# Kernel tuning notes

Measured on AMD Instinct MI355X. Metric: run time of the kernel, lower is better.

Reference implementation:

```python
import jax, jax.numpy as jnp
import numpy as np

BS = 256          # batch_size
NN = BS - 1
D = 128           # projection dim
SIGMA = 0.07      # rbf gamma (self.sigma)
C = 1.0
REG = 0.1
NUM_ITERS = 1000
ETA = 0.001
USE_NORM = True


def setup_inputs() -> dict:
    key = jax.random.key(0)
    k1, k2 = jax.random.split(key)
    z = jax.random.normal(k1, (BS, 2, D), dtype=jnp.float32)
    alpha_init = jax.random.normal(k2, (BS, NN, 1), dtype=jnp.float32)
    return {"z": z, "alpha_init": alpha_init}


def _rbf_kernel(X, Y, gamma):
    # exp(-gamma * ||x - y||^2)
    xn = jnp.sum(X * X, axis=1, keepdims=True)          # [n,1]
    yn = jnp.sum(Y * Y, axis=1, keepdims=True).T        # [1,m]
    d = xn + yn - 2.0 * (X @ Y.T)
    return jnp.exp(-gamma * d)


def _pgd_nesterov(DD, p, alpha0, eta, num_iters, C, use_norm):
    # minimize 0.5 a'DDa - p'a  s.t. 0 <= a <= C, batched over bs
    def step(carry, t):
        alpha, alpha_prev = carry
        beta = t / (t + 3.0)
        y = alpha + beta * (alpha - alpha_prev)
        grad = jnp.einsum('bij,bjk->bik', DD, y) - p     # [bs,nn,1]
        if use_norm:
            grad = grad / (jnp.linalg.norm(grad, axis=1, keepdims=True) + 1e-12)
        alpha_new = jnp.clip(y - eta * grad, 0.0, C)
        return (alpha_new, alpha), None
    (alpha, _), _ = jax.lax.scan(step, (alpha0, alpha0),
                                 jnp.arange(num_iters, dtype=jnp.float32))
    return alpha


def reference(z, alpha_init):
    bs, nn = BS, NN
    # F.normalize(z, p=2, dim=1): normalize over the view axis (faithful to source)
    nrm = jnp.maximum(jnp.linalg.norm(z, axis=1, keepdims=True), 1e-12)
    ftr = z / nrm
    ftr = jnp.concatenate([ftr[:, 0, :], ftr[:, 1, :]], axis=0)   # [2bs, d]

    K = _rbf_kernel(ftr[:bs], ftr, SIGMA)                          # [bs, 2bs]

    # ---- QP construction + solve under no_grad ----
    Kd = jax.lax.stop_gradient(K)
    KK = Kd[:, :bs]                                                # block: first bs cols
    r = jnp.arange(bs)
    m = jnp.arange(nn)
    # idx[i] = [0..bs-1] without i  (KMASK row/col removal)
    idx = m[None, :] + (m[None, :] >= r[:, None]).astype(jnp.int32)  # [bs, nn]
    KK_sub = KK[idx[:, :, None], idx[:, None, :]]                  # [bs,nn,nn]
    row = jnp.take_along_axis(KK, idx, axis=1)                     # row[i,m]=KK[i,idx[i,m]]
    # Delta[i,j,k] = 1 + reg*d_jk + KK[j,k] - KK[i,j] - KK[i,k]  (j,k != i)
    DD = (1.0 + REG * jnp.eye(nn, dtype=KK.dtype)[None]
          + KK_sub - row[:, :, None] - row[:, None, :])            # [bs,nn,nn]

    p = 2.0 * jnp.ones((bs, nn, 1), dtype=jnp.float32)
    alpha0 = jnp.clip(jax.nn.relu(alpha_init), 0.0, C)
    alpha = _pgd_nesterov(DD, p, alpha0, ETA, NUM_ITERS, C, USE_NORM)
    alpha_y = jnp.clip(jax.nn.relu(alpha[:, :, 0]), 0.0, C)
    alpha_y = jax.lax.stop_gradient(alpha_y)                       # [bs,nn]
    alpha_x = alpha_y.sum(axis=1)                                  # [bs]

    # ---- loss terms (grad flows through K here) ----
    Ks = K[:, bs:]                                                 # block12: [bs,bs]
    # Kn.T[i,m] = Ks.T[i, idx[i,m]]  (neg_mask = off-diagonal)
    KnT = jnp.take_along_axis(Ks.T, idx, axis=1)                   # [bs,nn]
    pos = jnp.diagonal(Ks)                                         # pos_mask = eye
    pos_loss = jnp.mean(alpha_x * pos)
    neg_loss = jnp.sum(alpha_y * KnT) / bs
    loss = neg_loss - pos_loss

    sparsity = ((alpha_y == C).sum().astype(jnp.float32)
                / ((alpha_y > 0).sum().astype(jnp.float32) + 1e-10))
    num_zero = (alpha_y == 0.0).mean()
    return (loss, pos.mean(), KnT.mean(), sparsity, num_zero, jnp.float32(0.0))
```

## Files before the change

kernel.cpp:

```cpp
#include <hip/hip_runtime.h>
#include <math.h>

#define BS   256
#define NN   255
#define DIM  128
#define GAMMA 0.07
#define NUM_ITERS 1000

typedef float v2f __attribute__((ext_vector_type(2)));

__device__ __forceinline__ double wred_d(double v) {
  #pragma unroll
  for (int k = 1; k < 64; k <<= 1) v += __shfl_xor(v, k, 64);
  return v;
}
__device__ __forceinline__ int wred_i(int v) {
  #pragma unroll
  for (int k = 1; k < 64; k <<= 1) v += __shfl_xor(v, k, 64);
  return v;
}

__device__ __forceinline__ float RLF(float v, int lane) {
  return __int_as_float(__builtin_amdgcn_readlane(__float_as_int(v), lane));
}

template <int CTRL, int RMASK>
__device__ __forceinline__ float dpp_add(float x) {
  int t = __builtin_amdgcn_update_dpp(0, __float_as_int(x), CTRL, RMASK, 0xf, true);
  return x + __int_as_float(t);
}
__device__ __forceinline__ float wred64_dpp(float x) {
  x = dpp_add<0x111, 0xf>(x);
  x = dpp_add<0x112, 0xf>(x);
  x = dpp_add<0x114, 0xf>(x);
  x = dpp_add<0x118, 0xf>(x);
  x = dpp_add<0x142, 0xa>(x);
  x = dpp_add<0x143, 0xc>(x);
  return RLF(x, 63);
}

__device__ __forceinline__ float rsq_nr(float x) {
  float r;
  asm("v_rsq_f32 %0, %1" : "=v"(r) : "v"(x));
  r = r * (1.5f - 0.5f * x * r * r);
  return r;
}

__device__ __forceinline__ void pk_fma(v2f& acc, const v2f& k, const v2f& y) {
  asm("v_pk_fma_f32 %0, %1, %2, %0" : "+v"(acc) : "v"(k), "v"(y));
}

__device__ __forceinline__ float4 add4(float4 a, float4 b) {
  float4 c; c.x = a.x + b.x; c.y = a.y + b.y; c.z = a.z + b.z; c.w = a.w + b.w;
  return c;
}

__global__ void k_ftr(const float* __restrict__ z, double* __restrict__ ftrT) {
  int b = blockIdx.x;
  int d = threadIdx.x;
  double z0 = (double)z[b * 256 + d];
  double z1 = (double)z[b * 256 + 128 + d];
  double n = sqrt(z0 * z0 + z1 * z1);
  n = fmax(n, 1e-12);
  ftrT[d * 512 + b]       = z0 / n;
  ftrT[d * 512 + 256 + b] = z1 / n;
}

__global__ void k_K(const double* __restrict__ ftrT, float* __restrict__ K,
                    double* __restrict__ pk_knt, double* __restrict__ pos_arr) {
  int i = blockIdx.x;
  int t = threadIdx.x;
  __shared__ double rowi[DIM];
  __shared__ double redd[4];
  if (t < DIM) rowi[t] = ftrT[t * 512 + i];
  __syncthreads();
  double xn = 0.0;
  #pragma unroll 8
  for (int d = 0; d < DIM; ++d) xn += rowi[d] * rowi[d];

  double knt_part = 0.0;
  #pragma unroll
  for (int h = 0; h < 2; ++h) {
    int j = t + h * 256;
    double dot = 0.0, sq = 0.0;
    #pragma unroll 8
    for (int d = 0; d < DIM; ++d) {
      double f = ftrT[d * 512 + j];
      dot += rowi[d] * f;
      sq  += f * f;
    }
    double dist = xn + sq - 2.0 * dot;
    double kv = exp(-GAMMA * dist);
    K[i * 512 + j] = (float)kv;
    if (h == 1) {
      if (j == 256 + i) pos_arr[i] = kv;
      else knt_part += kv;
    }
  }
  double w = wred_d(knt_part);
  if ((t & 63) == 0) redd[t >> 6] = w;
  __syncthreads();
  if (t == 0) pk_knt[i] = redd[0] + redd[1] + redd[2] + redd[3];
}

__global__ __launch_bounds__(512, 2) void k_pgd(
    const float* __restrict__ K, const float* __restrict__ alpha_init,
    double* __restrict__ neg_arr, double* __restrict__ sa_arr,
    int* __restrict__ cnt1, int* __restrict__ cntp, int* __restrict__ cnt0) {
  int r = blockIdx.x;
  int tid = threadIdx.x;
  int l = tid & 63;
  int rg = tid >> 6;

  __shared__ __align__(16) float ytil[BS];
  __shared__ __align__(16) float part[8][BS];
  __shared__ float S_lds[1];
  __shared__ float betat[1024];

  for (int i = tid; i < 1024; i += 512)
    betat[i] = (float)i / ((float)i + 3.0f);

  v2f kq[64];
  #pragma unroll
  for (int j = 0; j < 16; ++j) {
    float4 r0 = *(const float4*)&K[(32 * rg + 2 * j + 0) * 512 + 4 * l];
    float4 r1 = *(const float4*)&K[(32 * rg + 2 * j + 1) * 512 + 4 * l];
    kq[j].x      = r0.x; kq[j].y      = r1.x;
    kq[16 + j].x = r0.y; kq[16 + j].y = r1.y;
    kq[32 + j].x = r0.z; kq[32 + j].y = r1.z;
    kq[48 + j].x = r0.w; kq[48 + j].y = r1.w;
  }
  #pragma unroll
  for (int j = 0; j < 64; ++j)
    asm volatile("" : "+v"(kq[j]));

  float al[4], ap[4], yv[4], kv[4], rm2[4];
  if (rg == 0) {
    #pragma unroll
    for (int k = 0; k < 4; ++k) {
      int a = 4 * l + k;
      if (a == r) {
        al[k] = 0.f; ap[k] = 0.f; yv[k] = 0.f; kv[k] = 0.f; rm2[k] = 0.f;
      } else {
        int c = a - (a > r ? 1 : 0);
        float v = alpha_init[r * NN + c];
        v = fminf(fmaxf(v, 0.f), 1.f);
        al[k] = v; ap[k] = v; yv[k] = v;
        kv[k] = 1.0f - K[r * 512 + a];
        rm2[k] = 2.0f;
      }
    }
    float4 y4 = {yv[0], yv[1], yv[2], yv[3]};
    *(float4*)&ytil[4 * l] = y4;
  }
  __syncthreads();

  int rq = r >> 2, rc = r & 3;

  for (int it = 0; it < NUM_ITERS; ++it) {
    if (rg == 1) {
      float4 yq = *(const float4*)&ytil[4 * l];
      float Sv = wred64_dpp((yq.x + yq.y) + (yq.z + yq.w));
      if (l == 0) S_lds[0] = Sv;
    }
    const float4* yb = (const float4*)&ytil[32 * rg];
    v2f a0 = {0.f, 0.f}, a1 = {0.f, 0.f}, a2 = {0.f, 0.f}, a3 = {0.f, 0.f};
    #pragma unroll
    for (int jj = 0; jj < 8; ++jj) {
      float4 yq = yb[jj];
      v2f ylo = {yq.x, yq.y};
      v2f yhi = {yq.z, yq.w};
      pk_fma(a0, kq[2 * jj],      ylo); pk_fma(a0, kq[2 * jj + 1],      yhi);
      pk_fma(a1, kq[16 + 2 * jj], ylo); pk_fma(a1, kq[16 + 2 * jj + 1], yhi);
      pk_fma(a2, kq[32 + 2 * jj], ylo); pk_fma(a2, kq[32 + 2 * jj + 1], yhi);
      pk_fma(a3, kq[48 + 2 * jj], ylo); pk_fma(a3, kq[48 + 2 * jj + 1], yhi);
    }
    float4 accw = {a0.x + a0.y, a1.x + a1.y, a2.x + a2.y, a3.x + a3.y};
    *(float4*)&part[rg][4 * l] = accw;
    __syncthreads();

    if (rg == 0) {
      float4 q0 = *(const float4*)&part[0][4 * l];
      float4 q1 = *(const float4*)&part[1][4 * l];
      float4 q2 = *(const float4*)&part[2][4 * l];
      float4 q3 = *(const float4*)&part[3][4 * l];
      float4 q4 = *(const float4*)&part[4][4 * l];
      float4 q5 = *(const float4*)&part[5][4 * l];
      float4 q6 = *(const float4*)&part[6][4 * l];
      float4 q7 = *(const float4*)&part[7][4 * l];
      float4 gA = add4(add4(add4(q0, q1), add4(q2, q3)),
                       add4(add4(q4, q5), add4(q6, q7)));
      float grv = (rc == 0) ? gA.x : (rc == 1) ? gA.y : (rc == 2) ? gA.z : gA.w;
      float gr = RLF(grv, rq);
      float Sv = S_lds[0];
      float beta = betat[it + 1];
      float g[4];
      g[0] = (gA.x - gr) - rm2[0] + kv[0] * Sv + 0.1f * yv[0];
      g[1] = (gA.y - gr) - rm2[1] + kv[1] * Sv + 0.1f * yv[1];
      g[2] = (gA.z - gr) - rm2[2] + kv[2] * Sv + 0.1f * yv[2];
      g[3] = (gA.w - gr) - rm2[3] + kv[3] * Sv + 0.1f * yv[3];
      float n2 = wred64_dpp((g[0] * g[0] + g[1] * g[1]) + (g[2] * g[2] + g[3] * g[3]));
      float sinv = 0.001f * rsq_nr(n2);
      #pragma unroll
      for (int k = 0; k < 4; ++k) {
        float na = fminf(fmaxf(fmaf(-sinv, g[k], yv[k]), 0.f), 1.f);
        ap[k] = al[k];
        al[k] = na;
        yv[k] = fmaf(beta, na - ap[k], na);
      }
      float4 y4 = {yv[0], yv[1], yv[2], yv[3]};
      *(float4*)&ytil[4 * l] = y4;
    }
    __syncthreads();
  }

  if (rg == 0) {
    double nl = 0.0, sa = 0.0;
    int c1 = 0, cp = 0, cz = 0;
    #pragma unroll
    for (int k = 0; k < 4; ++k) {
      int a = 4 * l + k;
      if (a != r) {
        float kx = K[a * 512 + 256 + r];
        nl += (double)al[k] * (double)kx;
        sa += (double)al[k];
        c1 += (al[k] == 1.0f);
        cp += (al[k] > 0.0f);
        cz += (al[k] == 0.0f);
      }
    }
    nl = wred_d(nl); sa = wred_d(sa);
    c1 = wred_i(c1); cp = wred_i(cp); cz = wred_i(cz);
    if (l == 0) {
      neg_arr[r] = nl;
      sa_arr[r]  = sa;
      cnt1[r] = c1; cntp[r] = cp; cnt0[r] = cz;
    }
  }
}

__global__ void k_fin(const double* __restrict__ pk_knt, const double* __restrict__ pos_arr,
                      const double* __restrict__ neg_arr, const double* __restrict__ sa_arr,
                      const int* __restrict__ cnt1, const int* __restrict__ cntp,
                      const int* __restrict__ cnt0, float* __restrict__ out) {
  int t = threadIdx.x;
  __shared__ double rd[16];
  __shared__ int ri[12];
  double knt = pk_knt[t];
  double pos = pos_arr[t];
  double neg = neg_arr[t];
  double pl  = sa_arr[t] * pos_arr[t];
  int a1 = cnt1[t], ap = cntp[t], a0 = cnt0[t];
  knt = wred_d(knt); pos = wred_d(pos); neg = wred_d(neg); pl = wred_d(pl);
  a1 = wred_i(a1); ap = wred_i(ap); a0 = wred_i(a0);
  int w = t >> 6;
  if ((t & 63) == 0) {
    rd[w] = knt; rd[4 + w] = pos; rd[8 + w] = neg; rd[12 + w] = pl;
    ri[w] = a1; ri[4 + w] = ap; ri[8 + w] = a0;
  }
  __syncthreads();
  if (t == 0) {
    double kntS = rd[0] + rd[1] + rd[2] + rd[3];
    double posS = rd[4] + rd[5] + rd[6] + rd[7];
    double negS = rd[8] + rd[9] + rd[10] + rd[11];
    double plS  = rd[12] + rd[13] + rd[14] + rd[15];
    int c1t = ri[0] + ri[1] + ri[2] + ri[3];
    int cpt = ri[4] + ri[5] + ri[6] + ri[7];
    int c0t = ri[8] + ri[9] + ri[10] + ri[11];
    out[0] = (float)(negS / 256.0 - plS / 256.0);
    out[1] = (float)(posS / 256.0);
    out[2] = (float)(kntS / (256.0 * 255.0));
    out[3] = (float)c1t / ((float)cpt + 1e-10f);
    out[4] = (float)c0t / 65280.0f;
    out[5] = 0.0f;
  }
}

extern "C" void kernel_launch(void* const* d_in, const int* in_sizes, int n_in,
                              void* d_out, int out_size, void* d_ws, size_t ws_size,
                              hipStream_t stream) {
  const float* z     = (const float*)d_in[0];
  const float* ainit = (const float*)d_in[1];
  char* ws = (char*)d_ws;
  double* ftrT   = (double*)ws;
  float*  K      = (float*)(ws + 524288);
  double* pk_knt = (double*)(ws + 1048576);
  double* pos_a  = (double*)(ws + 1048576 + 2048);
  double* neg_a  = (double*)(ws + 1048576 + 4096);
  double* sa_a   = (double*)(ws + 1048576 + 6144);
  int* cnt1 = (int*)(ws + 1048576 + 8192);
  int* cntp = (int*)(ws + 1048576 + 8192 + 1024);
  int* cnt0 = (int*)(ws + 1048576 + 8192 + 2048);
  float* out = (float*)d_out;

  k_ftr<<<256, 128, 0, stream>>>(z, ftrT);
  k_K  <<<256, 256, 0, stream>>>(ftrT, K, pk_knt, pos_a);
  k_pgd<<<256, 512, 0, stream>>>(K, ainit, neg_a, sa_a, cnt1, cntp, cnt0);
  k_fin<<<1, 256, 0, stream>>>(pk_knt, pos_a, neg_a, sa_a, cnt1, cntp, cnt0, out);
}
```

Before: 815.8 us.

## Replicate PGD update across all waves to drop second barrier per iteration

Every wave now redundantly computes the full gradient, norm and Nesterov update, instead of only wave 0 doing it. Each wave writes only the 32-element y slice it needs for its own matvec into a private LDS buffer. The partial-sum buffer is double-buffered so one __syncthreads per iteration is enough, removing the second barrier and the separate wave that computed the sum of y. The cost is redundant ALU work and LDS reads in all eight waves.

```diff
diff --git a/kernel.cpp b/kernel.cpp
--- a/kernel.cpp
+++ b/kernel.cpp
@@ -112,9 +112,8 @@
   int l = tid & 63;
   int rg = tid >> 6;
 
-  __shared__ __align__(16) float ytil[BS];
-  __shared__ __align__(16) float part[8][BS];
-  __shared__ float S_lds[1];
+  __shared__ __align__(16) float part[2][8][BS];
+  __shared__ __align__(16) float ywave[8][32];
   __shared__ float betat[1024];
 
   for (int i = tid; i < 1024; i += 512)
@@ -135,35 +134,32 @@
     asm volatile("" : "+v"(kq[j]));
 
   float al[4], ap[4], yv[4], kv[4], rm2[4];
-  if (rg == 0) {
-    #pragma unroll
-    for (int k = 0; k < 4; ++k) {
-      int a = 4 * l + k;
-      if (a == r) {
-        al[k] = 0.f; ap[k] = 0.f; yv[k] = 0.f; kv[k] = 0.f; rm2[k] = 0.f;
-      } else {
-        int c = a - (a > r ? 1 : 0);
-        float v = alpha_init[r * NN + c];
-        v = fminf(fmaxf(v, 0.f), 1.f);
-        al[k] = v; ap[k] = v; yv[k] = v;
-        kv[k] = 1.0f - K[r * 512 + a];
-        rm2[k] = 2.0f;
-      }
-    }
+  #pragma unroll
+  for (int k = 0; k < 4; ++k) {
+    int a = 4 * l + k;
+    if (a == r) {
+      al[k] = 0.f; ap[k] = 0.f; yv[k] = 0.f; kv[k] = 0.f; rm2[k] = 0.f;
+    } else {
+      int c = a - (a > r ? 1 : 0);
+      float v = alpha_init[r * NN + c];
+      v = fminf(fmaxf(v, 0.f), 1.f);
+      al[k] = v; ap[k] = v; yv[k] = v;
+      kv[k] = 1.0f - K[r * 512 + a];
+      rm2[k] = 2.0f;
+    }
+  }
+  if ((l >> 3) == rg) {
     float4 y4 = {yv[0], yv[1], yv[2], yv[3]};
-    *(float4*)&ytil[4 * l] = y4;
+    *(float4*)&ywave[rg][4 * (l & 7)] = y4;
   }
   __syncthreads();
 
   int rq = r >> 2, rc = r & 3;
 
   for (int it = 0; it < NUM_ITERS; ++it) {
-    if (rg == 1) {
-      float4 yq = *(const float4*)&ytil[4 * l];
-      float Sv = wred64_dpp((yq.x + yq.y) + (yq.z + yq.w));
-      if (l == 0) S_lds[0] = Sv;
-    }
-    const float4* yb = (const float4*)&ytil[32 * rg];
+    float (*pb)[BS] = part[it & 1];
+
+    const float4* yb = (const float4*)&ywave[rg][0];
     v2f a0 = {0.f, 0.f}, a1 = {0.f, 0.f}, a2 = {0.f, 0.f}, a3 = {0.f, 0.f};
     #pragma unroll
     for (int jj = 0; jj < 8; ++jj) {
@@ -176,42 +172,41 @@
       pk_fma(a3, kq[48 + 2 * jj], ylo); pk_fma(a3, kq[48 + 2 * jj + 1], yhi);
     }
     float4 accw = {a0.x + a0.y, a1.x + a1.y, a2.x + a2.y, a3.x + a3.y};
-    *(float4*)&part[rg][4 * l] = accw;
+    *(float4*)&pb[rg][4 * l] = accw;
     __syncthreads();
 
-    if (rg == 0) {
-      float4 q0 = *(const float4*)&part[0][4 * l];
-      float4 q1 = *(const float4*)&part[1][4 * l];
-      float4 q2 = *(const float4*)&part[2][4 * l];
-      float4 q3 = *(const float4*)&part[3][4 * l];
-      float4 q4 = *(const float4*)&part[4][4 * l];
-      float4 q5 = *(const float4*)&part[5][4 * l];
-      float4 q6 = *(const float4*)&part[6][4 * l];
-      float4 q7 = *(const float4*)&part[7][4 * l];
-      float4 gA = add4(add4(add4(q0, q1), add4(q2, q3)),
-                       add4(add4(q4, q5), add4(q6, q7)));
-      float grv = (rc == 0) ? gA.x : (rc == 1) ? gA.y : (rc == 2) ? gA.z : gA.w;
-      float gr = RLF(grv, rq);
-      float Sv = S_lds[0];
-      float beta = betat[it + 1];
-      float g[4];
-      g[0] = (gA.x - gr) - rm2[0] + kv[0] * Sv + 0.1f * yv[0];
-      g[1] = (gA.y - gr) - rm2[1] + kv[1] * Sv + 0.1f * yv[1];
-      g[2] = (gA.z - gr) - rm2[2] + kv[2] * Sv + 0.1f * yv[2];
-      g[3] = (gA.w - gr) - rm2[3] + kv[3] * Sv + 0.1f * yv[3];
-      float n2 = wred64_dpp((g[0] * g[0] + g[1] * g[1]) + (g[2] * g[2] + g[3] * g[3]));
-      float sinv = 0.001f * rsq_nr(n2);
-      #pragma unroll
-      for (int k = 0; k < 4; ++k) {
-        float na = fminf(fmaxf(fmaf(-sinv, g[k], yv[k]), 0.f), 1.f);
-        ap[k] = al[k];
-        al[k] = na;
-        yv[k] = fmaf(beta, na - ap[k], na);
-      }
+    float4 q0 = *(const float4*)&pb[0][4 * l];
+    float4 q1 = *(const float4*)&pb[1][4 * l];
+    float4 q2 = *(const float4*)&pb[2][4 * l];
+    float4 q3 = *(const float4*)&pb[3][4 * l];
+    float4 q4 = *(const float4*)&pb[4][4 * l];
+    float4 q5 = *(const float4*)&pb[5][4 * l];
+    float4 q6 = *(const float4*)&pb[6][4 * l];
+    float4 q7 = *(const float4*)&pb[7][4 * l];
+    float4 gA = add4(add4(add4(q0, q1), add4(q2, q3)),
+                     add4(add4(q4, q5), add4(q6, q7)));
+    float grv = (rc == 0) ? gA.x : (rc == 1) ? gA.y : (rc == 2) ? gA.z : gA.w;
+    float gr = RLF(grv, rq);
+    float Sv = wred64_dpp((yv[0] + yv[1]) + (yv[2] + yv[3]));
+    float beta = betat[it + 1];
+    float g[4];
+    g[0] = (gA.x - gr) - rm2[0] + kv[0] * Sv + 0.1f * yv[0];
+    g[1] = (gA.y - gr) - rm2[1] + kv[1] * Sv + 0.1f * yv[1];
+    g[2] = (gA.z - gr) - rm2[2] + kv[2] * Sv + 0.1f * yv[2];
+    g[3] = (gA.w - gr) - rm2[3] + kv[3] * Sv + 0.1f * yv[3];
+    float n2 = wred64_dpp((g[0] * g[0] + g[1] * g[1]) + (g[2] * g[2] + g[3] * g[3]));
+    float sinv = 0.001f * rsq_nr(n2);
+    #pragma unroll
+    for (int k = 0; k < 4; ++k) {
+      float na = fminf(fmaxf(fmaf(-sinv, g[k], yv[k]), 0.f), 1.f);
+      ap[k] = al[k];
+      al[k] = na;
+      yv[k] = fmaf(beta, na - ap[k], na);
+    }
+    if ((l >> 3) == rg) {
       float4 y4 = {yv[0], yv[1], yv[2], yv[3]};
-      *(float4*)&ytil[4 * l] = y4;
-    }
-    __syncthreads();
+      *(float4*)&ywave[rg][4 * (l & 7)] = y4;
+    }
   }
 
   if (rg == 0) {
```

New measurement: 912.2 us. +11.8%, slower.

## Split PGD matvec across 16 waves with halved per-thread register tiles

Applied to the files above, without the earlier changes.

The PGD kernel now launches 1024 threads per block instead of 512. Each wave holds half the columns of a 32-row block of K, so per-thread resident K values drop from 128 floats to 64 and the per-iteration FMA chain shortens. The remove-mask constant is computed inline rather than kept in a register array, and the partial-sum adds are interleaved with the LDS loads. In exchange, each iteration's block-wide barriers now synchronise twice as many waves while the serial reduction in wave 0 stays the same.

```diff
diff --git a/kernel.cpp b/kernel.cpp
--- a/kernel.cpp
+++ b/kernel.cpp
@@ -103,51 +103,50 @@
   if (t == 0) pk_knt[i] = redd[0] + redd[1] + redd[2] + redd[3];
 }
 
-__global__ __launch_bounds__(512, 2) void k_pgd(
+__global__ __launch_bounds__(1024, 4) void k_pgd(
     const float* __restrict__ K, const float* __restrict__ alpha_init,
     double* __restrict__ neg_arr, double* __restrict__ sa_arr,
     int* __restrict__ cnt1, int* __restrict__ cntp, int* __restrict__ cnt0) {
   int r = blockIdx.x;
   int tid = threadIdx.x;
   int l = tid & 63;
-  int rg = tid >> 6;
+  int w = tid >> 6;
+  int rg = w & 7;
+  int h  = w >> 3;
+  int cb = 128 * h + 2 * l;
 
   __shared__ __align__(16) float ytil[BS];
   __shared__ __align__(16) float part[8][BS];
   __shared__ float S_lds[1];
   __shared__ float betat[1024];
 
-  for (int i = tid; i < 1024; i += 512)
-    betat[i] = (float)i / ((float)i + 3.0f);
-
-  v2f kq[64];
+  betat[tid] = (float)tid / ((float)tid + 3.0f);
+
+  v2f kq[32];
   #pragma unroll
   for (int j = 0; j < 16; ++j) {
-    float4 r0 = *(const float4*)&K[(32 * rg + 2 * j + 0) * 512 + 4 * l];
-    float4 r1 = *(const float4*)&K[(32 * rg + 2 * j + 1) * 512 + 4 * l];
+    float2 r0 = *(const float2*)&K[(32 * rg + 2 * j + 0) * 512 + cb];
+    float2 r1 = *(const float2*)&K[(32 * rg + 2 * j + 1) * 512 + cb];
     kq[j].x      = r0.x; kq[j].y      = r1.x;
     kq[16 + j].x = r0.y; kq[16 + j].y = r1.y;
-    kq[32 + j].x = r0.z; kq[32 + j].y = r1.z;
-    kq[48 + j].x = r0.w; kq[48 + j].y = r1.w;
-  }
-  #pragma unroll
-  for (int j = 0; j < 64; ++j)
+  }
+  #pragma unroll
+  for (int j = 0; j < 32; ++j)
     asm volatile("" : "+v"(kq[j]));
 
-  float al[4], ap[4], yv[4], kv[4], rm2[4];
-  if (rg == 0) {
+  float al[4], ap[4], yv[4], kv[4];
+  if (w == 0) {
     #pragma unroll
     for (int k = 0; k < 4; ++k) {
       int a = 4 * l + k;
       if (a == r) {
-        al[k] = 0.f; ap[k] = 0.f; yv[k] = 0.f; kv[k] = 0.f; rm2[k] = 0.f;
+        al[k] = 0.f; ap[k] = 0.f; yv[k] = 0.f; kv[k] = 0.f;
       } else {
         int c = a - (a > r ? 1 : 0);
         float v = alpha_init[r * NN + c];
         v = fminf(fmaxf(v, 0.f), 1.f);
         al[k] = v; ap[k] = v; yv[k] = v;
         kv[k] = 1.0f - K[r * 512 + a];
-        rm2[k] = 2.0f;
       }
     }
     float4 y4 = {yv[0], yv[1], yv[2], yv[3]};
@@ -158,13 +157,13 @@
   int rq = r >> 2, rc = r & 3;
 
   for (int it = 0; it < NUM_ITERS; ++it) {
-    if (rg == 1) {
+    if (w == 1) {
       float4 yq = *(const float4*)&ytil[4 * l];
       float Sv = wred64_dpp((yq.x + yq.y) + (yq.z + yq.w));
       if (l == 0) S_lds[0] = Sv;
     }
     const float4* yb = (const float4*)&ytil[32 * rg];
-    v2f a0 = {0.f, 0.f}, a1 = {0.f, 0.f}, a2 = {0.f, 0.f}, a3 = {0.f, 0.f};
+    v2f a0 = {0.f, 0.f}, a1 = {0.f, 0.f};
     #pragma unroll
     for (int jj = 0; jj < 8; ++jj) {
       float4 yq = yb[jj];
@@ -172,33 +171,37 @@
       v2f yhi = {yq.z, yq.w};
       pk_fma(a0, kq[2 * jj],      ylo); pk_fma(a0, kq[2 * jj + 1],      yhi);
       pk_fma(a1, kq[16 + 2 * jj], ylo); pk_fma(a1, kq[16 + 2 * jj + 1], yhi);
-      pk_fma(a2, kq[32 + 2 * jj], ylo); pk_fma(a2, kq[32 + 2 * jj + 1], yhi);
-      pk_fma(a3, kq[48 + 2 * jj], ylo); pk_fma(a3, kq[48 + 2 * jj + 1], yhi);
-    }
-    float4 accw = {a0.x + a0.y, a1.x + a1.y, a2.x + a2.y, a3.x + a3.y};
-    *(float4*)&part[rg][4 * l] = accw;
+    }
+    float2 accw = {a0.x + a0.y, a1.x + a1.y};
+    *(float2*)&part[rg][cb] = accw;
     __syncthreads();
 
-    if (rg == 0) {
+    if (w == 0) {
       float4 q0 = *(const float4*)&part[0][4 * l];
       float4 q1 = *(const float4*)&part[1][4 * l];
+      float4 s01 = add4(q0, q1);
       float4 q2 = *(const float4*)&part[2][4 * l];
       float4 q3 = *(const float4*)&part[3][4 * l];
+      float4 s23 = add4(q2, q3);
+      float4 sA = add4(s01, s23);
       float4 q4 = *(const float4*)&part[4][4 * l];
       float4 q5 = *(const float4*)&part[5][4 * l];
+      float4 s45 = add4(q4, q5);
       float4 q6 = *(const float4*)&part[6][4 * l];
       float4 q7 = *(const float4*)&part[7][4 * l];
-      float4 gA = add4(add4(add4(q0, q1), add4(q2, q3)),
-                       add4(add4(q4, q5), add4(q6, q7)));
+      float4 s67 = add4(q6, q7);
+      float4 gA = add4(sA, add4(s45, s67));
       float grv = (rc == 0) ? gA.x : (rc == 1) ? gA.y : (rc == 2) ? gA.z : gA.w;
       float gr = RLF(grv, rq);
       float Sv = S_lds[0];
       float beta = betat[it + 1];
       float g[4];
-      g[0] = (gA.x - gr) - rm2[0] + kv[0] * Sv + 0.1f * yv[0];
-      g[1] = (gA.y - gr) - rm2[1] + kv[1] * Sv + 0.1f * yv[1];
-      g[2] = (gA.z - gr) - rm2[2] + kv[2] * Sv + 0.1f * yv[2];
-      g[3] = (gA.w - gr) - rm2[3] + kv[3] * Sv + 0.1f * yv[3];
+      #pragma unroll
+      for (int k = 0; k < 4; ++k) {
+        float rm = (4 * l + k == r) ? 0.f : 2.f;
+        float gc = (k == 0) ? gA.x : (k == 1) ? gA.y : (k == 2) ? gA.z : gA.w;
+        g[k] = (gc - gr) - rm + kv[k] * Sv + 0.1f * yv[k];
+      }
       float n2 = wred64_dpp((g[0] * g[0] + g[1] * g[1]) + (g[2] * g[2] + g[3] * g[3]));
       float sinv = 0.001f * rsq_nr(n2);
       #pragma unroll
@@ -214,7 +217,7 @@
     __syncthreads();
   }
 
-  if (rg == 0) {
+  if (w == 0) {
     double nl = 0.0, sa = 0.0;
     int c1 = 0, cp = 0, cz = 0;
     #pragma unroll
@@ -295,6 +298,6 @@
 
   k_ftr<<<256, 128, 0, stream>>>(z, ftrT);
   k_K  <<<256, 256, 0, stream>>>(ftrT, K, pk_knt, pos_a);
-  k_pgd<<<256, 512, 0, stream>>>(K, ainit, neg_a, sa_a, cnt1, cntp, cnt0);
+  k_pgd<<<256, 1024, 0, stream>>>(K, ainit, neg_a, sa_a, cnt1, cntp, cnt0);
   k_fin<<<1, 256, 0, stream>>>(pk_knt, pos_a, neg_a, sa_a, cnt1, cntp, cnt0, out);
 }
```

Result: slower. 844.0 us (+3.5%).
